# Optimization experiments

Measured on AMD Instinct MI355X. Metric: run time of the kernel, lower is better.

Reference implementation:

```python
import jax, jax.numpy as jnp
import numpy as np

V, E, H, L = 50257, 1024, 1024, 512


def setup_inputs() -> dict:
    key = jax.random.key(0)
    ks = jax.random.split(key, 12)
    s = 0.02
    return {
        'input': jax.random.randint(ks[0], (1,), 0, V),
        'hidden': jax.random.normal(ks[1], (1, 1, H), dtype=jnp.float32),
        'encoder_outputs': jax.random.normal(ks[2], (L, H), dtype=jnp.float32),
        'emb_table': jax.random.normal(ks[3], (V, E), dtype=jnp.float32) * s,
        'attn_W': jax.random.normal(ks[4], (L, E + H), dtype=jnp.float32) * s,
        'attn_b': jax.random.normal(ks[5], (L,), dtype=jnp.float32) * s,
        'W_ih': jax.random.normal(ks[6], (3 * H, E + H), dtype=jnp.float32) * s,
        'W_hh': jax.random.normal(ks[7], (3 * H, H), dtype=jnp.float32) * s,
        'b_ih': jax.random.normal(ks[8], (3 * H,), dtype=jnp.float32) * s,
        'b_hh': jax.random.normal(ks[9], (3 * H,), dtype=jnp.float32) * s,
        'out_W': jax.random.normal(ks[10], (V, H), dtype=jnp.float32) * s,
        'out_b': jax.random.normal(ks[11], (V,), dtype=jnp.float32) * s,
    }


def reference(input, hidden, encoder_outputs, emb_table, attn_W, attn_b,
              W_ih, W_hh, b_ih, b_hh, out_W, out_b):
    # Dropout is inference-identity here.
    embedded = emb_table[input].reshape(1, E)                      # [1, E]
    h = hidden[0]                                                  # [1, H]
    attn_in = jnp.concatenate([embedded, h], axis=1)               # [1, E+H]
    attn_weights = jax.nn.softmax(attn_in @ attn_W.T + attn_b, axis=1)  # [1, L]
    attn_applied = attn_weights @ encoder_outputs                  # [1, H]
    x = jnp.concatenate([embedded, attn_applied], axis=1)          # [1, E+H]
    # PyTorch GRU cell, gate order (r, z, n)
    gi = x @ W_ih.T + b_ih                                         # [1, 3H]
    gh = h @ W_hh.T + b_hh                                         # [1, 3H]
    i_r, i_z, i_n = gi[:, :H], gi[:, H:2 * H], gi[:, 2 * H:]
    h_r, h_z, h_n = gh[:, :H], gh[:, H:2 * H], gh[:, 2 * H:]
    r = jax.nn.sigmoid(i_r + h_r)
    z = jax.nn.sigmoid(i_z + h_z)
    n = jnp.tanh(i_n + r * h_n)
    h_new = (1.0 - z) * n + z * h                                  # [1, H]
    log_probs = jax.nn.log_softmax(h_new @ out_W.T + out_b, axis=1)  # [1, V]
    return log_probs, h_new[None], attn_weights
```

## Files before the change

### kernel.cpp

```cpp
#include <hip/hip_runtime.h>
#include <math.h>

#define V 50257
#define E 1024
#define H 1024
#define L 512

#define OUT_H  50257
#define OUT_AW 51281

#define WS_S    0
#define WS_X    1024
#define WS_GH   3072
#define WS_GI   6144
#define WS_BM   10240
#define WS_BS   12288

__device__ __forceinline__ float dot4(const float4 a, const float4 b) {
    return a.x * b.x + a.y * b.y + a.z * b.z + a.w * b.w;
}

__device__ __forceinline__ float wave_sum(float v) {
    for (int off = 32; off > 0; off >>= 1) v += __shfl_down(v, off, 64);
    return v;
}

__global__ void k1_scores_gh(const int* __restrict__ input,
                             const float* __restrict__ hidden,
                             const float* __restrict__ emb_table,
                             const float* __restrict__ attn_W,
                             const float* __restrict__ attn_b,
                             const float* __restrict__ W_hh,
                             const float* __restrict__ b_hh,
                             float* __restrict__ ws) {
    const int t = threadIdx.x;
    const int lane = t & 63;
    const int gwave = blockIdx.x * 4 + (t >> 6);
    const float4* h4 = (const float4*)hidden;
    const float* embrow = emb_table + (size_t)input[0] * E;

    if (gwave < L) {
        const float4* emb4 = (const float4*)embrow;
        const float4* w4 = (const float4*)(attn_W + (size_t)gwave * (E + H));
        float acc = 0.f;
#pragma unroll
        for (int k = 0; k < 8; ++k) {
            int i = lane + 64 * k;
            float4 a = (k < 4) ? emb4[i] : h4[i - E / 4];
            acc += dot4(a, w4[i]);
        }
        acc = wave_sum(acc);
        if (lane == 0) ws[WS_S + gwave] = acc + attn_b[gwave];
    } else if (gwave < L + 3 * H) {
        int k = gwave - L;
        const float4* w4 = (const float4*)(W_hh + (size_t)k * H);
        float acc = 0.f;
#pragma unroll
        for (int ii = 0; ii < 4; ++ii) {
            int i = lane + 64 * ii;
            acc += dot4(h4[i], w4[i]);
        }
        acc = wave_sum(acc);
        if (lane == 0) ws[WS_GH + k] = acc + b_hh[k];
    } else if (gwave < 3600) {
        ws[WS_X + E + (gwave - 3584) * 64 + lane] = 0.f;
    } else if (gwave < 3616) {
        int i = (gwave - 3600) * 64 + lane;
        ws[WS_X + i] = embrow[i];
    }
}

__global__ void k2_softmax_applied(const float* __restrict__ enc,
                                   float* __restrict__ ws,
                                   float* __restrict__ out) {
    __shared__ float w[512];
    __shared__ float redm[4], reds[4];
    __shared__ float bmax, bsum;
    const int t = threadIdx.x;
    const int lane = t & 63, wid = t >> 6;

    float v0 = ws[WS_S + t];
    float v1 = ws[WS_S + 256 + t];
    float m = fmaxf(v0, v1);
    for (int off = 32; off > 0; off >>= 1) m = fmaxf(m, __shfl_down(m, off, 64));
    if (lane == 0) redm[wid] = m;
    __syncthreads();
    if (t == 0) bmax = fmaxf(fmaxf(redm[0], redm[1]), fmaxf(redm[2], redm[3]));
    __syncthreads();
    float e0 = expf(v0 - bmax), e1 = expf(v1 - bmax);
    float s = wave_sum(e0 + e1);
    if (lane == 0) reds[wid] = s;
    __syncthreads();
    if (t == 0) bsum = reds[0] + reds[1] + reds[2] + reds[3];
    __syncthreads();
    float inv = 1.f / bsum;
    w[t] = e0 * inv;
    w[256 + t] = e1 * inv;
    if (blockIdx.x == 0) {
        out[OUT_AW + t] = e0 * inv;
        out[OUT_AW + 256 + t] = e1 * inv;
    }
    __syncthreads();

    const int j = (blockIdx.x & 3) * 256 + t;
    const int l0 = (blockIdx.x >> 2) * 16;
    float acc = 0.f;
#pragma unroll
    for (int l = l0; l < l0 + 16; ++l)
        acc += w[l] * enc[(size_t)l * H + j];
    atomicAdd(&ws[WS_X + E + j], acc);
}

__global__ void k3_gi(const float* __restrict__ W_ih, const float* __restrict__ b_ih,
                      float* __restrict__ ws) {
    const int lane = threadIdx.x & 63;
    const int gwave = blockIdx.x * 4 + (threadIdx.x >> 6);
    const float4* x4 = (const float4*)(ws + WS_X);
    const float4* w4 = (const float4*)(W_ih + (size_t)gwave * (E + H));
    float acc = 0.f;
#pragma unroll
    for (int k = 0; k < 8; ++k) {
        int i = lane + 64 * k;
        acc += dot4(x4[i], w4[i]);
    }
    acc = wave_sum(acc);
    if (lane == 0) ws[WS_GI + gwave] = acc + b_ih[gwave];
}

__global__ void k4_logits(const float* __restrict__ hidden,
                          const float* __restrict__ out_W,
                          const float* __restrict__ out_b,
                          float* __restrict__ ws,
                          float* __restrict__ out) {
    __shared__ float hn[H];
    __shared__ float wm[4], wsum[4];
    const int t = threadIdx.x;
    const int lane = t & 63, wid = t >> 6;
    const int gwave = blockIdx.x * 4 + wid;

    const float4* w4_0 = (const float4*)(out_W + (size_t)gwave * H);
    float4 pre0 = w4_0[lane];
    float4 pre1 = w4_0[lane + 64];
    float4 pre2 = w4_0[lane + 128];
    float4 pre3 = w4_0[lane + 192];

#pragma unroll
    for (int c = 0; c < 4; ++c) {
        int k = t + 256 * c;
        float gir = ws[WS_GI + k],         ghr = ws[WS_GH + k];
        float giz = ws[WS_GI + H + k],     ghz = ws[WS_GH + H + k];
        float gin = ws[WS_GI + 2 * H + k], ghn = ws[WS_GH + 2 * H + k];
        float r = 1.f / (1.f + expf(-(gir + ghr)));
        float z = 1.f / (1.f + expf(-(giz + ghz)));
        float n = tanhf(gin + r * ghn);
        float v = (1.f - z) * n + z * hidden[k];
        hn[k] = v;
        if (blockIdx.x == 0) out[OUT_H + k] = v;
    }
    __syncthreads();

    const float4* hn4 = (const float4*)hn;
    float4 h0 = hn4[lane];
    float4 h1 = hn4[lane + 64];
    float4 h2 = hn4[lane + 128];
    float4 h3 = hn4[lane + 192];

    float m = -INFINITY, s = 0.f;

    {
        float acc = dot4(h0, pre0) + dot4(h1, pre1) + dot4(h2, pre2) + dot4(h3, pre3);
        acc = wave_sum(acc);
        if (lane == 0) {
            float lg = acc + out_b[gwave];
            out[gwave] = lg;
            m = lg; s = 1.f;
        }
    }
    for (int row = gwave + 8192; row < V; row += 8192) {
        const float4* w4 = (const float4*)(out_W + (size_t)row * H);
        float acc = dot4(h0, w4[lane])
                  + dot4(h1, w4[lane + 64])
                  + dot4(h2, w4[lane + 128])
                  + dot4(h3, w4[lane + 192]);
        acc = wave_sum(acc);
        if (lane == 0) {
            float lg = acc + out_b[row];
            out[row] = lg;
            if (lg > m) { s = s * expf(m - lg) + 1.f; m = lg; }
            else        { s += expf(lg - m); }
        }
    }
    if (lane == 0) { wm[wid] = m; wsum[wid] = s; }
    __syncthreads();
    if (t == 0) {
        float M = fmaxf(fmaxf(wm[0], wm[1]), fmaxf(wm[2], wm[3]));
        float S = wsum[0] * expf(wm[0] - M) + wsum[1] * expf(wm[1] - M)
                + wsum[2] * expf(wm[2] - M) + wsum[3] * expf(wm[3] - M);
        ws[WS_BM + blockIdx.x] = M;
        ws[WS_BS + blockIdx.x] = S;
    }
}

__global__ void k5_logprobs(const float* __restrict__ ws, float* __restrict__ out) {
    __shared__ float redm[4], reds[4];
    __shared__ float off_s;
    const int t = threadIdx.x;
    const int lane = t & 63, wid = t >> 6;
    float m = -INFINITY, s = 0.f;
#pragma unroll
    for (int c = 0; c < 8; ++c) {
        int b = t + 256 * c;
        float bm = ws[WS_BM + b], bs = ws[WS_BS + b];
        float M2 = fmaxf(m, bm);
        s = s * expf(m - M2) + bs * expf(bm - M2);
        m = M2;
    }
    for (int off = 32; off > 0; off >>= 1) {
        float mo = __shfl_down(m, off, 64);
        float so = __shfl_down(s, off, 64);
        float M2 = fmaxf(m, mo);
        s = s * expf(m - M2) + so * expf(mo - M2);
        m = M2;
    }
    if (lane == 0) { redm[wid] = m; reds[wid] = s; }
    __syncthreads();
    if (t == 0) {
        float M = redm[0], S = reds[0];
        for (int i = 1; i < 4; ++i) {
            float M2 = fmaxf(M, redm[i]);
            S = S * expf(M - M2) + reds[i] * expf(redm[i] - M2);
            M = M2;
        }
        off_s = M + logf(S);
    }
    __syncthreads();
    int i = blockIdx.x * 256 + t;
    if (i < V) out[i] -= off_s;
}

extern "C" void kernel_launch(void* const* d_in, const int* in_sizes, int n_in,
                              void* d_out, int out_size, void* d_ws, size_t ws_size,
                              hipStream_t stream) {
    const int*   input   = (const int*)d_in[0];
    const float* hidden  = (const float*)d_in[1];
    const float* enc     = (const float*)d_in[2];
    const float* emb     = (const float*)d_in[3];
    const float* attn_W  = (const float*)d_in[4];
    const float* attn_b  = (const float*)d_in[5];
    const float* W_ih    = (const float*)d_in[6];
    const float* W_hh    = (const float*)d_in[7];
    const float* b_ih    = (const float*)d_in[8];
    const float* b_hh    = (const float*)d_in[9];
    const float* out_W   = (const float*)d_in[10];
    const float* out_b   = (const float*)d_in[11];
    float* out = (float*)d_out;
    float* ws  = (float*)d_ws;

    k1_scores_gh<<<904, 256, 0, stream>>>(input, hidden, emb, attn_W, attn_b, W_hh, b_hh, ws);
    k2_softmax_applied<<<128, 256, 0, stream>>>(enc, ws, out);
    k3_gi<<<768, 256, 0, stream>>>(W_ih, b_ih, ws);
    k4_logits<<<2048, 256, 0, stream>>>(hidden, out_W, out_b, ws, out);
    k5_logprobs<<<197, 256, 0, stream>>>(ws, out);
}
```

Baseline: 420.9 us.

## Prefetch next out_W row in logits, halve grid, fold softmax exp into scores

The logits kernel now runs 1024 blocks with a fixed per-wave row count. It double-buffers the next out_W row in registers so the load overlaps the current dot product, and gathers the biases with one per-lane load plus shuffles. The attention softmax drops its max-subtraction: scores are exponentiated in k1 and summed with a global atomic, which removes the block reductions from k2 but adds a memset and an overflow risk. The k5 reduction loop shrinks to match the new block count.

```diff
diff --git a/kernel.cpp b/kernel.cpp
--- a/kernel.cpp
+++ b/kernel.cpp
@@ -10,6 +10,7 @@
 #define OUT_AW 51281
 
 #define WS_S    0
+#define WS_SUM  512
 #define WS_X    1024
 #define WS_GH   3072
 #define WS_GI   6144
@@ -50,7 +51,11 @@
             acc += dot4(a, w4[i]);
         }
         acc = wave_sum(acc);
-        if (lane == 0) ws[WS_S + gwave] = acc + attn_b[gwave];
+        if (lane == 0) {
+            float e = expf(acc + attn_b[gwave]);
+            ws[WS_S + gwave] = e;
+            atomicAdd(&ws[WS_SUM], e);
+        }
     } else if (gwave < L + 3 * H) {
         int k = gwave - L;
         const float4* w4 = (const float4*)(W_hh + (size_t)k * H);
@@ -74,31 +79,16 @@
                                    float* __restrict__ ws,
                                    float* __restrict__ out) {
     __shared__ float w[512];
-    __shared__ float redm[4], reds[4];
-    __shared__ float bmax, bsum;
-    const int t = threadIdx.x;
-    const int lane = t & 63, wid = t >> 6;
-
-    float v0 = ws[WS_S + t];
-    float v1 = ws[WS_S + 256 + t];
-    float m = fmaxf(v0, v1);
-    for (int off = 32; off > 0; off >>= 1) m = fmaxf(m, __shfl_down(m, off, 64));
-    if (lane == 0) redm[wid] = m;
-    __syncthreads();
-    if (t == 0) bmax = fmaxf(fmaxf(redm[0], redm[1]), fmaxf(redm[2], redm[3]));
-    __syncthreads();
-    float e0 = expf(v0 - bmax), e1 = expf(v1 - bmax);
-    float s = wave_sum(e0 + e1);
-    if (lane == 0) reds[wid] = s;
-    __syncthreads();
-    if (t == 0) bsum = reds[0] + reds[1] + reds[2] + reds[3];
-    __syncthreads();
-    float inv = 1.f / bsum;
-    w[t] = e0 * inv;
-    w[256 + t] = e1 * inv;
+    const int t = threadIdx.x;
+
+    float inv = 1.f / ws[WS_SUM];
+    float w0 = ws[WS_S + t] * inv;
+    float w1 = ws[WS_S + 256 + t] * inv;
+    w[t] = w0;
+    w[256 + t] = w1;
     if (blockIdx.x == 0) {
-        out[OUT_AW + t] = e0 * inv;
-        out[OUT_AW + 256 + t] = e1 * inv;
+        out[OUT_AW + t] = w0;
+        out[OUT_AW + 256 + t] = w1;
     }
     __syncthreads();
 
@@ -127,22 +117,26 @@
     if (lane == 0) ws[WS_GI + gwave] = acc + b_ih[gwave];
 }
 
-__global__ void k4_logits(const float* __restrict__ hidden,
-                          const float* __restrict__ out_W,
-                          const float* __restrict__ out_b,
-                          float* __restrict__ ws,
-                          float* __restrict__ out) {
+__global__ __launch_bounds__(256, 4)
+void k4_logits(const float* __restrict__ hidden,
+               const float* __restrict__ out_W,
+               const float* __restrict__ out_b,
+               float* __restrict__ ws,
+               float* __restrict__ out) {
     __shared__ float hn[H];
     __shared__ float wm[4], wsum[4];
     const int t = threadIdx.x;
     const int lane = t & 63, wid = t >> 6;
     const int gwave = blockIdx.x * 4 + wid;
+    const int nrows = 12 + (gwave < (V - 12 * 4096));
 
     const float4* w4_0 = (const float4*)(out_W + (size_t)gwave * H);
-    float4 pre0 = w4_0[lane];
-    float4 pre1 = w4_0[lane + 64];
-    float4 pre2 = w4_0[lane + 128];
-    float4 pre3 = w4_0[lane + 192];
+    float4 c0 = w4_0[lane];
+    float4 c1 = w4_0[lane + 64];
+    float4 c2 = w4_0[lane + 128];
+    float4 c3 = w4_0[lane + 192];
+
+    float ob = (lane < nrows) ? out_b[gwave + lane * 4096] : 0.f;
 
 #pragma unroll
     for (int c = 0; c < 4; ++c) {
@@ -166,29 +160,27 @@
     float4 h3 = hn4[lane + 192];
 
     float m = -INFINITY, s = 0.f;
-
-    {
-        float acc = dot4(h0, pre0) + dot4(h1, pre1) + dot4(h2, pre2) + dot4(h3, pre3);
+    for (int k = 0; k < nrows; ++k) {
+        const int row = gwave + k * 4096;
+        float4 n0, n1, n2, n3;
+        const bool more = (k + 1 < nrows);
+        if (more) {
+            const float4* nx = (const float4*)(out_W + (size_t)(row + 4096) * H);
+            n0 = nx[lane];
+            n1 = nx[lane + 64];
+            n2 = nx[lane + 128];
+            n3 = nx[lane + 192];
+        }
+        float acc = dot4(h0, c0) + dot4(h1, c1) + dot4(h2, c2) + dot4(h3, c3);
         acc = wave_sum(acc);
+        float obk = __shfl(ob, k, 64);
         if (lane == 0) {
-            float lg = acc + out_b[gwave];
-            out[gwave] = lg;
-            m = lg; s = 1.f;
-        }
-    }
-    for (int row = gwave + 8192; row < V; row += 8192) {
-        const float4* w4 = (const float4*)(out_W + (size_t)row * H);
-        float acc = dot4(h0, w4[lane])
-                  + dot4(h1, w4[lane + 64])
-                  + dot4(h2, w4[lane + 128])
-                  + dot4(h3, w4[lane + 192]);
-        acc = wave_sum(acc);
-        if (lane == 0) {
-            float lg = acc + out_b[row];
+            float lg = acc + obk;
             out[row] = lg;
             if (lg > m) { s = s * expf(m - lg) + 1.f; m = lg; }
             else        { s += expf(lg - m); }
         }
+        if (more) { c0 = n0; c1 = n1; c2 = n2; c3 = n3; }
     }
     if (lane == 0) { wm[wid] = m; wsum[wid] = s; }
     __syncthreads();
@@ -208,7 +200,7 @@
     const int lane = t & 63, wid = t >> 6;
     float m = -INFINITY, s = 0.f;
 #pragma unroll
-    for (int c = 0; c < 8; ++c) {
+    for (int c = 0; c < 4; ++c) {
         int b = t + 256 * c;
         float bm = ws[WS_BM + b], bs = ws[WS_BS + b];
         float M2 = fmaxf(m, bm);
@@ -256,9 +248,11 @@
     float* out = (float*)d_out;
     float* ws  = (float*)d_ws;
 
+    hipMemsetAsync((char*)d_ws + WS_SUM * sizeof(float), 0, sizeof(float), stream);
+
     k1_scores_gh<<<904, 256, 0, stream>>>(input, hidden, emb, attn_W, attn_b, W_hh, b_hh, ws);
     k2_softmax_applied<<<128, 256, 0, stream>>>(enc, ws, out);
     k3_gi<<<768, 256, 0, stream>>>(W_ih, b_ih, ws);
-    k4_logits<<<2048, 256, 0, stream>>>(hidden, out_W, out_b, ws, out);
+    k4_logits<<<1024, 256, 0, stream>>>(hidden, out_W, out_b, ws, out);
     k5_logprobs<<<197, 256, 0, stream>>>(ws, out);
 }
```

Result: no change. 426.9 us (+1.4%).
